# Kernel optimization log

Measured on AMD Instinct MI355X. Metric: run time of the kernel, lower is better.

## Reference

```python
import jax, jax.numpy as jnp
import numpy as np

B, T, S, H = 16, 1024, 1024, 512  # batch, dec len, src len, hidden


def setup_inputs() -> dict:
    key = jax.random.key(0)
    k1, k2, k3, k4 = jax.random.split(key, 4)
    decoder_output = jax.random.normal(k1, (B, T, H), dtype=jnp.float32)
    context = jax.random.normal(k2, (B, S, 2 * H), dtype=jnp.float32)
    mask = jax.random.randint(k3, (B, T, S), 0, 2) > 0  # bool
    # nn.Linear(2H, H, bias=False) weight: [H, 2H]
    W_a = jax.random.normal(k4, (H, 2 * H), dtype=jnp.float32) * (1.0 / np.sqrt(2 * H))
    return {"decoder_output": decoder_output, "context": context, "mask": mask, "W_a": W_a}


def reference(decoder_output, context, mask, W_a):
    # context_in = W_a(context).transpose(1, 2): [B, H, S]
    context_in = jnp.einsum('bsc,hc->bhs', context, W_a)
    # scores: [B, T, S]
    scores = jnp.einsum('bth,bhs->bts', decoder_output, context_in)
    scores = jnp.where(mask, jnp.float32(-1000000.0), scores)
    attn = jax.nn.softmax(scores, axis=2)
    # weighted sum over source: [B, T, 2H]
    weighted_sum = jnp.einsum('bts,bsc->btc', attn, context)
    return weighted_sum
```

## Files before the change

kernel.cpp:

```cpp
#include <hip/hip_runtime.h>
#include <cstdint>
#include <cstddef>


constexpr int BB = 16;
constexpr int TT = 1024;
constexpr int SS = 1024;
constexpr int HH = 512;

typedef __attribute__((ext_vector_type(8))) short short8v;
typedef __attribute__((ext_vector_type(4))) float f32x4;

__device__ inline unsigned short f2bf(float x) {
    unsigned int u = __float_as_uint(x);
    return (unsigned short)((u + 0x7FFFu + ((u >> 16) & 1u)) >> 16);
}
__device__ inline float bf2f(unsigned short h) {
    return __uint_as_float(((unsigned int)h) << 16);
}
__device__ inline void gload16(const void* g, void* l) {
    __builtin_amdgcn_global_load_lds(
        (const __attribute__((address_space(1))) unsigned int*)g,
        (__attribute__((address_space(3))) unsigned int*)l, 16, 0, 0);
}

__global__ __launch_bounds__(256)
void detect_mask(const unsigned char* __restrict__ mask, int* __restrict__ flag) {
    __shared__ int cnt;
    if (threadIdx.x == 0) cnt = 0;
    __syncthreads();
    int c = 0;
    for (int i = threadIdx.x; i < 4096; i += 256)
        if ((i & 3) != 0 && mask[i] != 0) c++;
    atomicAdd(&cnt, c);
    __syncthreads();
    if (threadIdx.x == 0) *flag = (cnt > 0) ? 1 : 0;
}

__global__ __launch_bounds__(256)
void split_pack(const float* __restrict__ in, unsigned short* __restrict__ oh,
                unsigned short* __restrict__ ol, int K, int KT, long sIn, long sOut)
{
    in += (size_t)blockIdx.z * sIn;
    oh += (size_t)blockIdx.z * sOut;
    ol += (size_t)blockIdx.z * sOut;
    const int rt = blockIdx.x / KT, kt = blockIdx.x % KT;
    const size_t tileBase = (size_t)blockIdx.x * 4096;
    #pragma unroll
    for (int s = 0; s < 2; ++s) {
        const int u  = threadIdx.x + (s << 8);
        const int r  = ((u >> 6) << 4) + (u & 15);
        const int k8 = ((u >> 4) & 3) << 3;
        const float* src = in + (size_t)(rt * 128 + r) * K + kt * 32 + k8;
        const float4 x = *(const float4*)src;
        const float4 y = *(const float4*)(src + 4);
        const float v[8] = {x.x, x.y, x.z, x.w, y.x, y.y, y.z, y.w};
        short8v H, L;
        #pragma unroll
        for (int j = 0; j < 8; ++j) {
            const unsigned short h = f2bf(v[j]);
            H[j] = (short)h;
            L[j] = (short)f2bf(v[j] - bf2f(h));
        }
        *(short8v*)(oh + tileBase + (size_t)u * 8) = H;
        *(short8v*)(ol + tileBase + (size_t)u * 8) = L;
    }
}

__global__ __launch_bounds__(256)
void pack_bf16(const unsigned short* __restrict__ in, unsigned short* __restrict__ op,
               int K, int KT, long sIn, long sOut)
{
    in += (size_t)blockIdx.z * sIn;
    op += (size_t)blockIdx.z * sOut;
    const int rt = blockIdx.x / KT, kt = blockIdx.x % KT;
    const size_t tileBase = (size_t)blockIdx.x * 4096;
    #pragma unroll
    for (int s = 0; s < 2; ++s) {
        const int u  = threadIdx.x + (s << 8);
        const int r  = ((u >> 6) << 4) + (u & 15);
        const int k8 = ((u >> 4) & 3) << 3;
        const short8v v = *(const short8v*)(in + (size_t)(rt * 128 + r) * K + kt * 32 + k8);
        *(short8v*)(op + tileBase + (size_t)u * 8) = v;
    }
}

__global__ __launch_bounds__(256)
void transpose_pack(const float* __restrict__ src, unsigned short* __restrict__ dst,
                    long sIn, long sOut)
{
    __shared__ float t[32][132];
    src += (size_t)blockIdx.z * sIn;
    dst += (size_t)blockIdx.z * sOut;
    const int c0 = blockIdx.x << 7, s0 = blockIdx.y << 5;
    #pragma unroll
    for (int i = 0; i < 4; ++i) {
        const int fl = threadIdx.x + (i << 8);
        const int srow = fl >> 5, c4 = fl & 31;
        const float4 v = *(const float4*)(src + (size_t)(s0 + srow) * (2 * HH) + c0 + (c4 << 2));
        t[srow][(c4 << 2) + 0] = v.x;
        t[srow][(c4 << 2) + 1] = v.y;
        t[srow][(c4 << 2) + 2] = v.z;
        t[srow][(c4 << 2) + 3] = v.w;
    }
    __syncthreads();
    const size_t tileBase = ((size_t)blockIdx.x * (SS / 32) + blockIdx.y) * 4096;
    #pragma unroll
    for (int s = 0; s < 2; ++s) {
        const int u = threadIdx.x + (s << 8);
        const int r = ((u >> 6) << 4) + (u & 15);
        const int o = (u >> 4) & 3;
        short8v H;
        #pragma unroll
        for (int e = 0; e < 8; ++e)
            H[e] = (short)f2bf(t[(o << 3) + e][r]);
        *(short8v*)(dst + tileBase + (size_t)u * 8) = H;
    }
}

template <bool SPLIT>
__global__ __launch_bounds__(256, 2)
void gemm2_x3(const unsigned short* __restrict__ Ah, const unsigned short* __restrict__ Al,
              const unsigned short* __restrict__ Bh, const unsigned short* __restrict__ Bl,
              float* __restrict__ C, unsigned short* __restrict__ CH,
              unsigned short* __restrict__ CL,
              int N, int KTn, long sA, long sB, long sC)
{
    const int bz = blockIdx.z;
    const int tid = threadIdx.x, lane = tid & 63, wv = tid >> 6;
    const int wr = wv >> 1, wc = wv & 1;
    const int bx = blockIdx.x, by = blockIdx.y;

    __shared__ short sm[2][4][4096];

    const unsigned short* base =
        (wv == 0) ? Ah + (size_t)bz * sA : (wv == 1) ? Al + (size_t)bz * sA
      : (wv == 2) ? Bh + (size_t)bz * sB :            Bl + (size_t)bz * sB;
    const unsigned short* gsrc = base
        + (size_t)((wv < 2) ? bx : by) * KTn * 4096 + (size_t)lane * 8;

    f32x4 acc[4][4];
    #pragma unroll
    for (int i = 0; i < 4; ++i)
        #pragma unroll
        for (int j = 0; j < 4; ++j)
            acc[i][j] = (f32x4)(0.0f);

    #pragma unroll
    for (int f = 0; f < 8; ++f)
        gload16(gsrc + f * 512, &sm[0][wv][f * 512]);
    __syncthreads();

    int cur = 0;
    for (int kt = 0; kt < KTn; ++kt) {
        if (kt + 1 < KTn) {
            const unsigned short* g = gsrc + (size_t)(kt + 1) * 4096;
            #pragma unroll
            for (int f = 0; f < 8; ++f)
                gload16(g + f * 512, &sm[cur ^ 1][wv][f * 512]);
        }
        short8v ah[4], al[4], bh[4], bl[4];
        #pragma unroll
        for (int f = 0; f < 4; ++f) {
            const int fa = (((wr << 2) + f) * 64 + lane) * 8;
            const int fb = (((wc << 2) + f) * 64 + lane) * 8;
            ah[f] = *(const short8v*)&sm[cur][0][fa];
            al[f] = *(const short8v*)&sm[cur][1][fa];
            bh[f] = *(const short8v*)&sm[cur][2][fb];
            bl[f] = *(const short8v*)&sm[cur][3][fb];
        }
        #pragma unroll
        for (int i = 0; i < 4; ++i)
            #pragma unroll
            for (int j = 0; j < 4; ++j) {
                acc[i][j] = __builtin_amdgcn_mfma_f32_16x16x32_bf16(ah[i], bh[j], acc[i][j], 0, 0, 0);
                acc[i][j] = __builtin_amdgcn_mfma_f32_16x16x32_bf16(ah[i], bl[j], acc[i][j], 0, 0, 0);
                acc[i][j] = __builtin_amdgcn_mfma_f32_16x16x32_bf16(al[i], bh[j], acc[i][j], 0, 0, 0);
            }
        __syncthreads();
        cur ^= 1;
    }

    const int cr = (lane >> 4) << 2, cc = lane & 15;
    #pragma unroll
    for (int i = 0; i < 4; ++i) {
        const int row = (bx << 7) + (wr << 6) + (i << 4) + cr;
        #pragma unroll
        for (int j = 0; j < 4; ++j) {
            const int col = (by << 7) + (wc << 6) + (j << 4) + cc;
            #pragma unroll
            for (int r = 0; r < 4; ++r) {
                const size_t idx = (size_t)bz * sC + (size_t)(row + r) * N + col;
                const float v = acc[i][j][r];
                if (SPLIT) {
                    const unsigned short h = f2bf(v);
                    CH[idx] = h;
                    CL[idx] = f2bf(v - bf2f(h));
                } else {
                    C[idx] = v;
                }
            }
        }
    }
}

__global__ __launch_bounds__(256, 2)
void gemm2_x1(const unsigned short* __restrict__ A, const unsigned short* __restrict__ B,
              float* __restrict__ C, int N, int KTn, long sA, long sB, long sC)
{
    const int bz = blockIdx.z;
    const int tid = threadIdx.x, lane = tid & 63, wv = tid >> 6;
    const int wr = wv >> 1, wc = wv & 1;
    const int bx = blockIdx.x, by = blockIdx.y;

    __shared__ short sm[2][2][4096];

    const int half = wv & 1;
    const unsigned short* base = (wv < 2) ? A + (size_t)bz * sA : B + (size_t)bz * sB;
    const unsigned short* gsrc = base
        + (size_t)((wv < 2) ? bx : by) * KTn * 4096 + (size_t)(half * 4) * 512
        + (size_t)lane * 8;
    short* ldst = &sm[0][wv < 2 ? 0 : 1][half * 2048];

    f32x4 acc[4][4];
    #pragma unroll
    for (int i = 0; i < 4; ++i)
        #pragma unroll
        for (int j = 0; j < 4; ++j)
            acc[i][j] = (f32x4)(0.0f);

    #pragma unroll
    for (int f = 0; f < 4; ++f)
        gload16(gsrc + f * 512, ldst + f * 512);
    __syncthreads();

    int cur = 0;
    for (int kt = 0; kt < KTn; ++kt) {
        if (kt + 1 < KTn) {
            const unsigned short* g = gsrc + (size_t)(kt + 1) * 4096;
            short* l = &sm[cur ^ 1][wv < 2 ? 0 : 1][half * 2048];
            #pragma unroll
            for (int f = 0; f < 4; ++f)
                gload16(g + f * 512, l + f * 512);
        }
        short8v a[4], b[4];
        #pragma unroll
        for (int f = 0; f < 4; ++f) {
            a[f] = *(const short8v*)&sm[cur][0][(((wr << 2) + f) * 64 + lane) * 8];
            b[f] = *(const short8v*)&sm[cur][1][(((wc << 2) + f) * 64 + lane) * 8];
        }
        #pragma unroll
        for (int i = 0; i < 4; ++i)
            #pragma unroll
            for (int j = 0; j < 4; ++j)
                acc[i][j] = __builtin_amdgcn_mfma_f32_16x16x32_bf16(a[i], b[j], acc[i][j], 0, 0, 0);
        __syncthreads();
        cur ^= 1;
    }

    float* Cb = C + (size_t)bz * sC;
    const int cr = (lane >> 4) << 2, cc = lane & 15;
    #pragma unroll
    for (int i = 0; i < 4; ++i) {
        const int row = (bx << 7) + (wr << 6) + (i << 4) + cr;
        #pragma unroll
        for (int j = 0; j < 4; ++j) {
            const int col = (by << 7) + (wc << 6) + (j << 4) + cc;
            #pragma unroll
            for (int r = 0; r < 4; ++r)
                Cb[(size_t)(row + r) * N + col] = acc[i][j][r];
        }
    }
}

__global__ __launch_bounds__(256)
void softmax_mask_bf16(const float* __restrict__ attnF, unsigned short* __restrict__ attnB,
                       const unsigned char* __restrict__ maskg,
                       const int* __restrict__ maskMode, long rowOff)
{
    __shared__ float red[8];
    const long row = blockIdx.x;
    const float4* p = (const float4*)(attnF + row * (long)SS);
    float4 v = p[threadIdx.x];

    const long mrow = (rowOff + row) * (long)SS;
    if (*maskMode) {
        const uchar4 mk = ((const uchar4*)(maskg + mrow))[threadIdx.x];
        if (mk.x) v.x = -1000000.0f;
        if (mk.y) v.y = -1000000.0f;
        if (mk.z) v.z = -1000000.0f;
        if (mk.w) v.w = -1000000.0f;
    } else {
        const int4 mk = ((const int4*)((const int*)maskg + mrow))[threadIdx.x];
        if (mk.x) v.x = -1000000.0f;
        if (mk.y) v.y = -1000000.0f;
        if (mk.z) v.z = -1000000.0f;
        if (mk.w) v.w = -1000000.0f;
    }

    float m = fmaxf(fmaxf(v.x, v.y), fmaxf(v.z, v.w));
    #pragma unroll
    for (int off = 32; off; off >>= 1)
        m = fmaxf(m, __shfl_xor(m, off));
    const int wave = threadIdx.x >> 6;
    if ((threadIdx.x & 63) == 0) red[wave] = m;
    __syncthreads();
    m = fmaxf(fmaxf(red[0], red[1]), fmaxf(red[2], red[3]));

    v.x = __expf(v.x - m);
    v.y = __expf(v.y - m);
    v.z = __expf(v.z - m);
    v.w = __expf(v.w - m);

    float s = v.x + v.y + v.z + v.w;
    #pragma unroll
    for (int off = 32; off; off >>= 1)
        s += __shfl_xor(s, off);
    if ((threadIdx.x & 63) == 0) red[4 + wave] = s;
    __syncthreads();
    s = red[4] + red[5] + red[6] + red[7];

    const float inv = 1.0f / s;
    ushort4 o;
    o.x = f2bf(v.x * inv);
    o.y = f2bf(v.y * inv);
    o.z = f2bf(v.z * inv);
    o.w = f2bf(v.w * inv);
    *(ushort4*)(attnB + row * (long)SS + 4 * threadIdx.x) = o;
}

extern "C" void kernel_launch(void* const* d_in, const int* in_sizes, int n_in,
                              void* d_out, int out_size, void* d_ws, size_t ws_size,
                              hipStream_t stream)
{
    const float*         dec  = (const float*)d_in[0];
    const float*         ctx  = (const float*)d_in[1];
    const unsigned char* mask = (const unsigned char*)d_in[2];
    const float*         Wa   = (const float*)d_in[3];
    float* out = (float*)d_out;

    const size_t MBy = 1u << 20;
    const size_t perBatch = 12 * MBy;
    const size_t fixed = 256 + 2 * MBy;
    int G = (ws_size > fixed) ? (int)((ws_size - fixed) / perBatch) : 1;
    if (G > BB) G = BB;
    if (G < 1)  G = 1;

    char* p = (char*)d_ws;
    int* maskMode = (int*)p;                      p += 256;
    unsigned short* WaHP = (unsigned short*)p;    p += (size_t)HH * 2 * HH * 2;
    unsigned short* WaLP = (unsigned short*)p;    p += (size_t)HH * 2 * HH * 2;
    unsigned short* ctxHP = (unsigned short*)p;
    unsigned short* ctxLP = ctxHP + (size_t)G * SS * 2 * HH;
    float*          attnF = (float*)p;            p += (size_t)G * 4 * MBy;
    unsigned short* decHP = (unsigned short*)p;
    unsigned short* decLP = decHP + (size_t)G * TT * HH;
    unsigned short* attnB = (unsigned short*)p;   p += (size_t)G * 2 * MBy;
    unsigned short* cinH  = (unsigned short*)p;
    unsigned short* cinL  = cinH + (size_t)G * SS * HH;
    unsigned short* attnP = (unsigned short*)p;   p += (size_t)G * 2 * MBy;
    unsigned short* cinHP = (unsigned short*)p;
    unsigned short* cinLP = cinHP + (size_t)G * SS * HH;  p += (size_t)G * 2 * MBy;
    unsigned short* ctxTP = (unsigned short*)p;   p += (size_t)G * 2 * MBy;

    detect_mask<<<1, 256, 0, stream>>>(mask, maskMode);
    split_pack<<<dim3(4 * 32, 1, 1), 256, 0, stream>>>(
        Wa, WaHP, WaLP, 2 * HH, 32, 0L, 0L);

    for (int g0 = 0; g0 < BB; g0 += G) {
        const int Gn = (BB - g0 < G) ? (BB - g0) : G;
        const float* ctxg = ctx + (size_t)g0 * SS * 2 * HH;

        split_pack<<<dim3(8 * 32, 1, Gn), 256, 0, stream>>>(
            ctxg, ctxHP, ctxLP, 2 * HH, 32, (long)SS * 2 * HH, (long)SS * 2 * HH);
        split_pack<<<dim3(8 * 16, 1, Gn), 256, 0, stream>>>(
            dec + (size_t)g0 * TT * HH, decHP, decLP, HH, 16,
            (long)TT * HH, (long)TT * HH);
        transpose_pack<<<dim3(8, 32, Gn), 256, 0, stream>>>(
            ctxg, ctxTP, (long)SS * 2 * HH, (long)2 * HH * SS);

        gemm2_x3<true><<<dim3(8, 4, Gn), 256, 0, stream>>>(
            ctxHP, ctxLP, WaHP, WaLP, nullptr, cinH, cinL,
            HH, 32, (long)SS * 2 * HH, 0L, (long)SS * HH);

        pack_bf16<<<dim3(8 * 16, 1, Gn), 256, 0, stream>>>(
            cinH, cinHP, HH, 16, (long)SS * HH, (long)SS * HH);
        pack_bf16<<<dim3(8 * 16, 1, Gn), 256, 0, stream>>>(
            cinL, cinLP, HH, 16, (long)SS * HH, (long)SS * HH);

        gemm2_x3<false><<<dim3(8, 8, Gn), 256, 0, stream>>>(
            decHP, decLP, cinHP, cinLP, attnF, nullptr, nullptr,
            SS, 16, (long)TT * HH, (long)SS * HH, (long)TT * SS);

        softmax_mask_bf16<<<Gn * TT, 256, 0, stream>>>(
            attnF, attnB, mask, maskMode, (long)g0 * TT);

        pack_bf16<<<dim3(8 * 32, 1, Gn), 256, 0, stream>>>(
            attnB, attnP, SS, 32, (long)TT * SS, (long)TT * SS);

        gemm2_x1<<<dim3(8, 8, Gn), 256, 0, stream>>>(
            attnP, ctxTP, out + (size_t)g0 * TT * 2 * HH,
            2 * HH, 32, (long)TT * SS, (long)2 * HH * SS, (long)TT * 2 * HH);
    }
}
```

Before: 433.9 us.

## Fuse tile packing into GEMM and softmax epilogues; deepen LDS prefetch pipeline

Removes the three pack_bf16 launches. The first GEMM and the softmax kernel now write their outputs directly in the packed MFMA tile layout. Both GEMM kernels switch to a two-ahead prefetch scheme with explicit vmcnt waits and raw s_barrier instead of __syncthreads, so global-to-LDS loads overlap more compute. The packed-layout stores from the epilogues are scattered 2-byte and 8-byte writes, which may coalesce less well.

```diff
diff --git a/kernel.cpp b/kernel.cpp
--- a/kernel.cpp
+++ b/kernel.cpp
@@ -68,24 +68,6 @@
 }
 
 __global__ __launch_bounds__(256)
-void pack_bf16(const unsigned short* __restrict__ in, unsigned short* __restrict__ op,
-               int K, int KT, long sIn, long sOut)
-{
-    in += (size_t)blockIdx.z * sIn;
-    op += (size_t)blockIdx.z * sOut;
-    const int rt = blockIdx.x / KT, kt = blockIdx.x % KT;
-    const size_t tileBase = (size_t)blockIdx.x * 4096;
-    #pragma unroll
-    for (int s = 0; s < 2; ++s) {
-        const int u  = threadIdx.x + (s << 8);
-        const int r  = ((u >> 6) << 4) + (u & 15);
-        const int k8 = ((u >> 4) & 3) << 3;
-        const short8v v = *(const short8v*)(in + (size_t)(rt * 128 + r) * K + kt * 32 + k8);
-        *(short8v*)(op + tileBase + (size_t)u * 8) = v;
-    }
-}
-
-__global__ __launch_bounds__(256)
 void transpose_pack(const float* __restrict__ src, unsigned short* __restrict__ dst,
                     long sIn, long sOut)
 {
@@ -149,16 +131,17 @@
     #pragma unroll
     for (int f = 0; f < 8; ++f)
         gload16(gsrc + f * 512, &sm[0][wv][f * 512]);
-    __syncthreads();
-
-    int cur = 0;
+    #pragma unroll
+    for (int f = 0; f < 8; ++f)
+        gload16(gsrc + 4096 + f * 512, &sm[1][wv][f * 512]);
+
     for (int kt = 0; kt < KTn; ++kt) {
-        if (kt + 1 < KTn) {
-            const unsigned short* g = gsrc + (size_t)(kt + 1) * 4096;
-            #pragma unroll
-            for (int f = 0; f < 8; ++f)
-                gload16(g + f * 512, &sm[cur ^ 1][wv][f * 512]);
-        }
+        if (kt + 1 < KTn) asm volatile("s_waitcnt vmcnt(8)" ::: "memory");
+        else              asm volatile("s_waitcnt vmcnt(0)" ::: "memory");
+        __builtin_amdgcn_s_barrier();
+        __builtin_amdgcn_sched_barrier(0);
+        const int cur = kt & 1;
+
         short8v ah[4], al[4], bh[4], bl[4];
         #pragma unroll
         for (int f = 0; f < 4; ++f) {
@@ -177,28 +160,51 @@
                 acc[i][j] = __builtin_amdgcn_mfma_f32_16x16x32_bf16(ah[i], bl[j], acc[i][j], 0, 0, 0);
                 acc[i][j] = __builtin_amdgcn_mfma_f32_16x16x32_bf16(al[i], bh[j], acc[i][j], 0, 0, 0);
             }
-        __syncthreads();
-        cur ^= 1;
+
+        __builtin_amdgcn_s_barrier();
+        __builtin_amdgcn_sched_barrier(0);
+        if (kt + 2 < KTn) {
+            const unsigned short* g = gsrc + (size_t)(kt + 2) * 4096;
+            #pragma unroll
+            for (int f = 0; f < 8; ++f)
+                gload16(g + f * 512, &sm[cur][wv][f * 512]);
+        }
     }
 
     const int cr = (lane >> 4) << 2, cc = lane & 15;
-    #pragma unroll
-    for (int i = 0; i < 4; ++i) {
-        const int row = (bx << 7) + (wr << 6) + (i << 4) + cr;
-        #pragma unroll
-        for (int j = 0; j < 4; ++j) {
-            const int col = (by << 7) + (wc << 6) + (j << 4) + cc;
-            #pragma unroll
-            for (int r = 0; r < 4; ++r) {
-                const size_t idx = (size_t)bz * sC + (size_t)(row + r) * N + col;
-                const float v = acc[i][j][r];
-                if (SPLIT) {
+    if (SPLIT) {
+        const int KTt = N >> 5;
+        #pragma unroll
+        for (int i = 0; i < 4; ++i) {
+            const int frag = (wr << 2) + i;
+            #pragma unroll
+            for (int j = 0; j < 4; ++j) {
+                const int kt  = (by << 2) + (wc << 1) + (j >> 1);
+                const int oct = ((j & 1) << 1) + (cc >> 3);
+                const int e   = cc & 7;
+                #pragma unroll
+                for (int r = 0; r < 4; ++r) {
+                    const int l16 = cr + r;
+                    const size_t idx = (size_t)bz * sC
+                        + ((size_t)(bx * KTt + kt) << 12)
+                        + (size_t)(((frag << 6) + (oct << 4) + l16) << 3) + e;
+                    const float v = acc[i][j][r];
                     const unsigned short h = f2bf(v);
                     CH[idx] = h;
                     CL[idx] = f2bf(v - bf2f(h));
-                } else {
-                    C[idx] = v;
                 }
+            }
+        }
+    } else {
+        #pragma unroll
+        for (int i = 0; i < 4; ++i) {
+            const int row = (bx << 7) + (wr << 6) + (i << 4) + cr;
+            #pragma unroll
+            for (int j = 0; j < 4; ++j) {
+                const int col = (by << 7) + (wc << 6) + (j << 4) + cc;
+                #pragma unroll
+                for (int r = 0; r < 4; ++r)
+                    C[(size_t)bz * sC + (size_t)(row + r) * N + col] = acc[i][j][r];
             }
         }
     }
@@ -220,7 +226,7 @@
     const unsigned short* gsrc = base
         + (size_t)((wv < 2) ? bx : by) * KTn * 4096 + (size_t)(half * 4) * 512
         + (size_t)lane * 8;
-    short* ldst = &sm[0][wv < 2 ? 0 : 1][half * 2048];
+    const int arr = (wv < 2) ? 0 : 1;
 
     f32x4 acc[4][4];
     #pragma unroll
@@ -231,18 +237,18 @@
 
     #pragma unroll
     for (int f = 0; f < 4; ++f)
-        gload16(gsrc + f * 512, ldst + f * 512);
-    __syncthreads();
-
-    int cur = 0;
+        gload16(gsrc + f * 512, &sm[0][arr][half * 2048 + f * 512]);
+    #pragma unroll
+    for (int f = 0; f < 4; ++f)
+        gload16(gsrc + 4096 + f * 512, &sm[1][arr][half * 2048 + f * 512]);
+
     for (int kt = 0; kt < KTn; ++kt) {
-        if (kt + 1 < KTn) {
-            const unsigned short* g = gsrc + (size_t)(kt + 1) * 4096;
-            short* l = &sm[cur ^ 1][wv < 2 ? 0 : 1][half * 2048];
-            #pragma unroll
-            for (int f = 0; f < 4; ++f)
-                gload16(g + f * 512, l + f * 512);
-        }
+        if (kt + 1 < KTn) asm volatile("s_waitcnt vmcnt(4)" ::: "memory");
+        else              asm volatile("s_waitcnt vmcnt(0)" ::: "memory");
+        __builtin_amdgcn_s_barrier();
+        __builtin_amdgcn_sched_barrier(0);
+        const int cur = kt & 1;
+
         short8v a[4], b[4];
         #pragma unroll
         for (int f = 0; f < 4; ++f) {
@@ -254,8 +260,15 @@
             #pragma unroll
             for (int j = 0; j < 4; ++j)
                 acc[i][j] = __builtin_amdgcn_mfma_f32_16x16x32_bf16(a[i], b[j], acc[i][j], 0, 0, 0);
-        __syncthreads();
-        cur ^= 1;
+
+        __builtin_amdgcn_s_barrier();
+        __builtin_amdgcn_sched_barrier(0);
+        if (kt + 2 < KTn) {
+            const unsigned short* g = gsrc + (size_t)(kt + 2) * 4096;
+            #pragma unroll
+            for (int f = 0; f < 4; ++f)
+                gload16(g + f * 512, &sm[cur][arr][half * 2048 + f * 512]);
+        }
     }
 
     float* Cb = C + (size_t)bz * sC;
@@ -274,7 +287,7 @@
 }
 
 __global__ __launch_bounds__(256)
-void softmax_mask_bf16(const float* __restrict__ attnF, unsigned short* __restrict__ attnB,
+void softmax_mask_pack(const float* __restrict__ attnF, unsigned short* __restrict__ attnP,
                        const unsigned char* __restrict__ maskg,
                        const int* __restrict__ maskMode, long rowOff)
 {
@@ -326,7 +339,16 @@
     o.y = f2bf(v.y * inv);
     o.z = f2bf(v.z * inv);
     o.w = f2bf(v.w * inv);
-    *(ushort4*)(attnB + row * (long)SS + 4 * threadIdx.x) = o;
+
+    const int t = (int)(row & (TT - 1));
+    const int g = (int)(row >> 10);
+    const int s0 = threadIdx.x << 2;
+    const int rt = t >> 7, frag = (t >> 4) & 7, l16 = t & 15;
+    const int kt = s0 >> 5, oct = (s0 >> 3) & 3, e0 = s0 & 7;
+    const size_t idx = (size_t)g * TT * SS
+        + ((size_t)(rt * 32 + kt) << 12)
+        + (size_t)(((frag << 6) + (oct << 4) + l16) << 3) + e0;
+    *(ushort4*)(attnP + idx) = o;
 }
 
 extern "C" void kernel_launch(void* const* d_in, const int* in_sizes, int n_in,
@@ -355,9 +377,7 @@
     float*          attnF = (float*)p;            p += (size_t)G * 4 * MBy;
     unsigned short* decHP = (unsigned short*)p;
     unsigned short* decLP = decHP + (size_t)G * TT * HH;
-    unsigned short* attnB = (unsigned short*)p;   p += (size_t)G * 2 * MBy;
-    unsigned short* cinH  = (unsigned short*)p;
-    unsigned short* cinL  = cinH + (size_t)G * SS * HH;
+    p += (size_t)G * 2 * MBy;
     unsigned short* attnP = (unsigned short*)p;   p += (size_t)G * 2 * MBy;
     unsigned short* cinHP = (unsigned short*)p;
     unsigned short* cinLP = cinHP + (size_t)G * SS * HH;  p += (size_t)G * 2 * MBy;
@@ -380,23 +400,15 @@
             ctxg, ctxTP, (long)SS * 2 * HH, (long)2 * HH * SS);
 
         gemm2_x3<true><<<dim3(8, 4, Gn), 256, 0, stream>>>(
-            ctxHP, ctxLP, WaHP, WaLP, nullptr, cinH, cinL,
+            ctxHP, ctxLP, WaHP, WaLP, nullptr, cinHP, cinLP,
             HH, 32, (long)SS * 2 * HH, 0L, (long)SS * HH);
-
-        pack_bf16<<<dim3(8 * 16, 1, Gn), 256, 0, stream>>>(
-            cinH, cinHP, HH, 16, (long)SS * HH, (long)SS * HH);
-        pack_bf16<<<dim3(8 * 16, 1, Gn), 256, 0, stream>>>(
-            cinL, cinLP, HH, 16, (long)SS * HH, (long)SS * HH);
 
         gemm2_x3<false><<<dim3(8, 8, Gn), 256, 0, stream>>>(
             decHP, decLP, cinHP, cinLP, attnF, nullptr, nullptr,
             SS, 16, (long)TT * HH, (long)SS * HH, (long)TT * SS);
 
-        softmax_mask_bf16<<<Gn * TT, 256, 0, stream>>>(
-            attnF, attnB, mask, maskMode, (long)g0 * TT);
-
-        pack_bf16<<<dim3(8 * 32, 1, Gn), 256, 0, stream>>>(
-            attnB, attnP, SS, 32, (long)TT * SS, (long)TT * SS);
+        softmax_mask_pack<<<Gn * TT, 256, 0, stream>>>(
+            attnF, attnP, mask, maskMode, (long)g0 * TT);
 
         gemm2_x1<<<dim3(8, 8, Gn), 256, 0, stream>>>(
             attnP, ctxTP, out + (size_t)g0 * TT * 2 * HH,
```

New measurement: 415.5 us. 4.2% less time.
